# Kernel tuning notes

Measured on AMD Instinct MI355X. Metric: run time of the kernel, lower is better.

The kernel has to match this reference:

```python
import jax, jax.numpy as jnp
import numpy as np

D_MODEL, EDGE_DIM, HIDDEN = 128, 9, 256
B, N = 2, 512


def setup_inputs() -> dict:
    key = jax.random.key(0)
    ks = jax.random.split(key, 12)
    s = 0.05
    return {
        "z_prime": jax.random.normal(ks[0], (B, N, D_MODEL), jnp.float32),
        "edge_features": jax.random.normal(ks[1], (N, N, EDGE_DIM), jnp.float32),
        "candidate_edge_mask": jax.random.randint(ks[2], (N, N), 0, 2, jnp.int32),
        # organ head params (in, out) layout
        "Wo1": jax.random.normal(ks[3], (D_MODEL, HIDDEN), jnp.float32) * s,
        "bo1": jnp.zeros((HIDDEN,), jnp.float32),
        "Wo2": jax.random.normal(ks[4], (HIDDEN, 1), jnp.float32) * s,
        "bo2": jnp.zeros((1,), jnp.float32),
        # edge head first linear, split by input blocks [zi | zj | edge_feat]
        "We_i": jax.random.normal(ks[5], (D_MODEL, HIDDEN), jnp.float32) * s,
        "We_j": jax.random.normal(ks[6], (D_MODEL, HIDDEN), jnp.float32) * s,
        "We_e": jax.random.normal(ks[7], (EDGE_DIM, HIDDEN), jnp.float32) * s,
        "be1": jnp.zeros((HIDDEN,), jnp.float32),
        "We2": jax.random.normal(ks[8], (HIDDEN, 1), jnp.float32) * s,
        "be2": jnp.zeros((1,), jnp.float32),
    }


def reference(z_prime, edge_features, candidate_edge_mask,
              Wo1, bo1, Wo2, bo2, We_i, We_j, We_e, be1, We2, be2):
    # organ head: sigmoid(MLP(z)) -> (B, N)
    h_o = jax.nn.relu(jnp.einsum('bnd,dh->bnh', z_prime, Wo1) + bo1)
    organ_susceptibility = jax.nn.sigmoid(
        (jnp.einsum('bnh,ho->bno', h_o, Wo2) + bo2).squeeze(-1))

    # edge head: concat([zi, zj, E]) @ W1 decomposed into per-node/per-edge
    # projections (identical math to the concatenated linear).
    pi = jnp.einsum('bnd,dh->bnh', z_prime, We_i)   # (B, N, H) -> broadcast over j
    pj = jnp.einsum('bnd,dh->bnh', z_prime, We_j)   # (B, N, H) -> broadcast over i
    pe = jnp.einsum('ijd,dh->ijh', edge_features, We_e)  # (N, N, H)
    h = jax.nn.relu(pi[:, :, None, :] + pj[:, None, :, :] + pe[None] + be1)
    edge_prob = jax.nn.sigmoid(
        (jnp.einsum('bijh,ho->bijo', h, We2) + be2).squeeze(-1))
    edge_prob = edge_prob * candidate_edge_mask.astype(edge_prob.dtype)[None]
    return (organ_susceptibility, edge_prob)
```

## Files before the change

### kernel.cpp

```cpp
#include <hip/hip_runtime.h>
#include <math.h>
#include <stdint.h>

#define D_MODEL 128
#define EDGE_DIM 9
#define HIDDEN 256
#define BATCH 2
#define NN 512

#define TI 4
#define TJ 32

typedef _Float16 h2v    __attribute__((ext_vector_type(2)));
typedef __fp16   fp16x2 __attribute__((ext_vector_type(2)));
typedef _Float16 f16x8  __attribute__((ext_vector_type(8)));
typedef float    f32x4  __attribute__((ext_vector_type(4)));

struct H8 { h2v v[4]; };

__device__ __forceinline__ uint32_t h2u(h2v v) { return __builtin_bit_cast(uint32_t, v); }
__device__ __forceinline__ h2v u2h(uint32_t u) { return __builtin_bit_cast(h2v, u); }
__device__ __forceinline__ h2v pkrtz(float a, float b) {
    return __builtin_bit_cast(h2v, __builtin_amdgcn_cvt_pkrtz(a, b));
}
__device__ __forceinline__ h2v relu2(h2v v) {
    h2v z = {(_Float16)0.0f, (_Float16)0.0f};
    return __builtin_elementwise_max(v, z);
}
__device__ __forceinline__ float fdot2(h2v a, h2v b, float c) {
    return __builtin_amdgcn_fdot2(__builtin_bit_cast(fp16x2, a),
                                  __builtin_bit_cast(fp16x2, b), c, false);
}
__device__ __forceinline__ float sigmoidf_(float x) { return 1.f / (1.f + expf(-x)); }

__global__ __launch_bounds__(512) void node_mfma_kernel(
    const float* __restrict__ z,
    const float* __restrict__ Wo1,
    const float* __restrict__ bo1,
    const float* __restrict__ Wo2,
    const float* __restrict__ bo2,
    const float* __restrict__ We_i,
    const float* __restrict__ We_j,
    const float* __restrict__ be1,
    float* __restrict__ organ_out,
    uint32_t* __restrict__ pi_h,
    uint32_t* __restrict__ pj_h)
{
    __shared__ uint32_t Wlds[256][68];
    __shared__ float org_part[32][4];

    const int t    = threadIdx.x;
    const int lane = t & 63;
    const int wave = t >> 6;
    const int rb   = blockIdx.x;
    const int m    = blockIdx.y;

    const float* __restrict__ W = (m == 0) ? Wo1 : (m == 1) ? We_i : We_j;

    for (int idx = t; idx < 64 * 256; idx += 512) {
        const int d2 = idx >> 8;
        const int h  = idx & 255;
        const float wlo = W[(2 * d2) * 256 + h];
        const float whi = W[(2 * d2 + 1) * 256 + h];
        Wlds[h][d2 ^ ((h & 7) << 3)] = h2u(pkrtz(wlo, whi));
    }

    const int rt = wave & 1;
    const int cg = wave >> 1;
    const int kg = lane >> 4;
    const int row = rb * 32 + rt * 16 + (lane & 15);

    f16x8 A[4];
#pragma unroll
    for (int kt = 0; kt < 4; ++kt) {
        const float4 za = *(const float4*)&z[(size_t)row * 128 + kt * 32 + kg * 8];
        const float4 zb = *(const float4*)&z[(size_t)row * 128 + kt * 32 + kg * 8 + 4];
        H8 a;
        a.v[0] = pkrtz(za.x, za.y); a.v[1] = pkrtz(za.z, za.w);
        a.v[2] = pkrtz(zb.x, zb.y); a.v[3] = pkrtz(zb.z, zb.w);
        A[kt] = __builtin_bit_cast(f16x8, a);
    }

    __syncthreads();

    f32x4 C[4];
#pragma unroll
    for (int ct = 0; ct < 4; ++ct) {
        const int col = (cg * 4 + ct) * 16 + (lane & 15);
        C[ct] = (f32x4){0.f, 0.f, 0.f, 0.f};
#pragma unroll
        for (int kt = 0; kt < 4; ++kt) {
            const int d2b = (kt * 16 + kg * 4) ^ ((col & 7) << 3);
            const uint4 w = *(const uint4*)&Wlds[col][d2b];
            H8 b;
            b.v[0] = u2h(w.x); b.v[1] = u2h(w.y);
            b.v[2] = u2h(w.z); b.v[3] = u2h(w.w);
            C[ct] = __builtin_amdgcn_mfma_f32_16x16x32_f16(
                        A[kt], __builtin_bit_cast(f16x8, b), C[ct], 0, 0, 0);
        }
    }

    if (m == 0) {
        float s0 = 0.f, s1 = 0.f, s2 = 0.f, s3 = 0.f;
#pragma unroll
        for (int ct = 0; ct < 4; ++ct) {
            const int col = (cg * 4 + ct) * 16 + (lane & 15);
            const float b1 = bo1[col];
            const float w2 = Wo2[col];
            s0 = fmaf(fmaxf(C[ct].x + b1, 0.f), w2, s0);
            s1 = fmaf(fmaxf(C[ct].y + b1, 0.f), w2, s1);
            s2 = fmaf(fmaxf(C[ct].z + b1, 0.f), w2, s2);
            s3 = fmaf(fmaxf(C[ct].w + b1, 0.f), w2, s3);
        }
#pragma unroll
        for (int off = 1; off <= 8; off <<= 1) {
            s0 += __shfl_xor(s0, off, 64);
            s1 += __shfl_xor(s1, off, 64);
            s2 += __shfl_xor(s2, off, 64);
            s3 += __shfl_xor(s3, off, 64);
        }
        if ((lane & 15) == 0) {
            const int rbase = rt * 16 + kg * 4;
            org_part[rbase + 0][cg] = s0;
            org_part[rbase + 1][cg] = s1;
            org_part[rbase + 2][cg] = s2;
            org_part[rbase + 3][cg] = s3;
        }
        __syncthreads();
        if (t < 32) {
            const float s = org_part[t][0] + org_part[t][1]
                          + org_part[t][2] + org_part[t][3] + bo2[0];
            organ_out[rb * 32 + t] = sigmoidf_(s);
        }
    } else {
        uint32_t* __restrict__ dst = (m == 1) ? pi_h : pj_h;
        const bool addb = (m == 1);
#pragma unroll
        for (int ct = 0; ct < 4; ++ct) {
            const int col = (cg * 4 + ct) * 16 + (lane & 15);
            const float bv = addb ? be1[col] : 0.f;
            float v0 = C[ct].x + bv, v1 = C[ct].y + bv;
            float v2 = C[ct].z + bv, v3 = C[ct].w + bv;
            const float p0 = __shfl_xor(v0, 1, 64);
            const float p1 = __shfl_xor(v1, 1, 64);
            const float p2 = __shfl_xor(v2, 1, 64);
            const float p3 = __shfl_xor(v3, 1, 64);
            if (!(lane & 1)) {
                const int hp = col >> 1;
                const size_t gr = (size_t)(rb * 32 + rt * 16 + kg * 4);
                dst[(gr + 0) * 128 + hp] = h2u(pkrtz(v0, p0));
                dst[(gr + 1) * 128 + hp] = h2u(pkrtz(v1, p1));
                dst[(gr + 2) * 128 + hp] = h2u(pkrtz(v2, p2));
                dst[(gr + 3) * 128 + hp] = h2u(pkrtz(v3, p3));
            }
        }
    }
}

__global__ __launch_bounds__(256, 8) void edge_kernel(
    const float* __restrict__ E,
    const int*   __restrict__ mask,
    const float* __restrict__ We_e,
    const float* __restrict__ We2,
    const float* __restrict__ be2,
    const uint32_t* __restrict__ pi_h,
    const uint32_t* __restrict__ pj_h,
    float* __restrict__ edge_out)
{
    __shared__ __align__(16) uint32_t E_s[TI][TJ][12];
    __shared__ float sums_s[BATCH][TI][33];

    const int t    = threadIdx.x;
    const int lane = t & 63;
    const int wave = t >> 6;
    const int bi   = blockIdx.x;
    const int i0   = (bi >> 4) * TI;
    const int j0   = (bi & 15) * TJ;

#pragma unroll
    for (int ii = 0; ii < TI; ++ii) {
        const float* src = &E[((size_t)(i0 + ii) * NN + j0) * EDGE_DIM];
        for (int idx = t; idx < TJ * EDGE_DIM; idx += 256) {
            const int jl = idx / 9;
            const int d  = idx - jl * 9;
            const float e = src[idx];
            E_s[ii][jl][d] = h2u(pkrtz(e, e));
        }
    }

    h2v wee[EDGE_DIM][2];
    const float4* We_e4 = (const float4*)We_e;
#pragma unroll
    for (int d = 0; d < EDGE_DIM; ++d) {
        const float4 w = We_e4[d * 64 + lane];
        wee[d][0] = pkrtz(w.x, w.y);
        wee[d][1] = pkrtz(w.z, w.w);
    }
    h2v w2[2];
    {
        const float4 w = ((const float4*)We2)[lane];
        w2[0] = pkrtz(w.x, w.y);
        w2[1] = pkrtz(w.z, w.w);
    }

    h2v pir[BATCH][TI][2];
#pragma unroll
    for (int b = 0; b < BATCH; ++b)
#pragma unroll
        for (int ii = 0; ii < TI; ++ii) {
            const uint2 u = ((const uint2*)&pi_h[(size_t)(b * NN + i0 + ii) * 128])[lane];
            pir[b][ii][0] = u2h(u.x);
            pir[b][ii][1] = u2h(u.y);
        }

    __syncthreads();

    uint2 pjp[BATCH];
    {
        const int j = j0 + wave * 8;
        pjp[0] = ((const uint2*)&pj_h[(size_t)(0 * NN + j) * 128])[lane];
        pjp[1] = ((const uint2*)&pj_h[(size_t)(1 * NN + j) * 128])[lane];
    }

#pragma unroll
    for (int q = 0; q < 8; ++q) {
        const int jl = wave * 8 + q;

        h2v pjr[BATCH][2];
        pjr[0][0] = u2h(pjp[0].x); pjr[0][1] = u2h(pjp[0].y);
        pjr[1][0] = u2h(pjp[1].x); pjr[1][1] = u2h(pjp[1].y);

        if (q < 7) {
            const int j = j0 + jl + 1;
            pjp[0] = ((const uint2*)&pj_h[(size_t)(0 * NN + j) * 128])[lane];
            pjp[1] = ((const uint2*)&pj_h[(size_t)(1 * NN + j) * 128])[lane];
        }

        float vals[8];
#pragma unroll
        for (int ii = 0; ii < TI; ++ii) {
            const uint32_t* erow = &E_s[ii][jl][0];
            const uint4 ua = *(const uint4*)(erow);
            const uint4 ub = *(const uint4*)(erow + 4);
            const uint32_t uc = erow[8];

            h2v pe0, pe1;
            {
                const h2v e0 = u2h(ua.x), e1 = u2h(ua.y), e2 = u2h(ua.z), e3 = u2h(ua.w);
                const h2v e4 = u2h(ub.x), e5 = u2h(ub.y), e6 = u2h(ub.z), e7 = u2h(ub.w);
                const h2v e8 = u2h(uc);
                pe0 = e0 * wee[0][0];            pe1 = e0 * wee[0][1];
                pe0 = pe0 + e1 * wee[1][0];      pe1 = pe1 + e1 * wee[1][1];
                pe0 = pe0 + e2 * wee[2][0];      pe1 = pe1 + e2 * wee[2][1];
                pe0 = pe0 + e3 * wee[3][0];      pe1 = pe1 + e3 * wee[3][1];
                pe0 = pe0 + e4 * wee[4][0];      pe1 = pe1 + e4 * wee[4][1];
                pe0 = pe0 + e5 * wee[5][0];      pe1 = pe1 + e5 * wee[5][1];
                pe0 = pe0 + e6 * wee[6][0];      pe1 = pe1 + e6 * wee[6][1];
                pe0 = pe0 + e7 * wee[7][0];      pe1 = pe1 + e7 * wee[7][1];
                pe0 = pe0 + e8 * wee[8][0];      pe1 = pe1 + e8 * wee[8][1];
            }

#pragma unroll
            for (int b = 0; b < BATCH; ++b) {
                h2v v0 = relu2(pir[b][ii][0] + pjr[b][0] + pe0);
                h2v v1 = relu2(pir[b][ii][1] + pjr[b][1] + pe1);
                vals[2 * ii + b] = fdot2(v1, w2[1], fdot2(v0, w2[0], 0.f));
            }
        }

        float a0, a1, a2, a3;
        {
            const bool b0 = lane & 1;
            float k0 = b0 ? vals[1] : vals[0], s0 = b0 ? vals[0] : vals[1];
            float k1 = b0 ? vals[3] : vals[2], s1 = b0 ? vals[2] : vals[3];
            float k2 = b0 ? vals[5] : vals[4], s2 = b0 ? vals[4] : vals[5];
            float k3 = b0 ? vals[7] : vals[6], s3 = b0 ? vals[6] : vals[7];
            a0 = k0 + __shfl_xor(s0, 1, 64);
            a1 = k1 + __shfl_xor(s1, 1, 64);
            a2 = k2 + __shfl_xor(s2, 1, 64);
            a3 = k3 + __shfl_xor(s3, 1, 64);
        }
        {
            const bool b1 = (lane >> 1) & 1;
            float k0 = b1 ? a1 : a0, s0 = b1 ? a0 : a1;
            float k1 = b1 ? a3 : a2, s1 = b1 ? a2 : a3;
            a0 = k0 + __shfl_xor(s0, 2, 64);
            a1 = k1 + __shfl_xor(s1, 2, 64);
        }
        {
            const bool b2 = (lane >> 2) & 1;
            float k = b2 ? a1 : a0, s = b2 ? a0 : a1;
            a0 = k + __shfl_xor(s, 4, 64);
        }
        a0 += __shfl_xor(a0, 8, 64);
        a0 += __shfl_xor(a0, 16, 64);
        a0 += __shfl_xor(a0, 32, 64);

        if (lane < 8) sums_s[lane & 1][lane >> 1][jl] = a0;
    }
    __syncthreads();

    {
        const int b   = t >> 7;
        const int rem = t & 127;
        const int ii  = rem >> 5;
        const int jl  = rem & 31;
        const int i = i0 + ii, j = j0 + jl;
        const float s = sums_s[b][ii][jl] + be2[0];
        float p = sigmoidf_(s) * (float)mask[i * NN + j];
        edge_out[((size_t)b * NN + i) * NN + j] = p;
    }
}

extern "C" void kernel_launch(void* const* d_in, const int* in_sizes, int n_in,
                              void* d_out, int out_size, void* d_ws, size_t ws_size,
                              hipStream_t stream) {
    const float* z    = (const float*)d_in[0];
    const float* E    = (const float*)d_in[1];
    const int*   mask = (const int*)  d_in[2];
    const float* Wo1  = (const float*)d_in[3];
    const float* bo1  = (const float*)d_in[4];
    const float* Wo2  = (const float*)d_in[5];
    const float* bo2  = (const float*)d_in[6];
    const float* We_i = (const float*)d_in[7];
    const float* We_j = (const float*)d_in[8];
    const float* We_e = (const float*)d_in[9];
    const float* be1  = (const float*)d_in[10];
    const float* We2  = (const float*)d_in[11];
    const float* be2  = (const float*)d_in[12];

    float* out_organ = (float*)d_out;
    float* out_edge  = out_organ + BATCH * NN;

    uint32_t* pi_h = (uint32_t*)d_ws;
    uint32_t* pj_h = pi_h + (size_t)BATCH * NN * (HIDDEN/2);

    hipLaunchKernelGGL(node_mfma_kernel,
                       dim3(32, 3), dim3(512), 0, stream,
                       z, Wo1, bo1, Wo2, bo2, We_i, We_j, be1,
                       out_organ, pi_h, pj_h);

    hipLaunchKernelGGL(edge_kernel,
                       dim3((NN / TI) * (NN / TJ)), dim3(256), 0, stream,
                       E, mask, We_e, We2, be2, pi_h, pj_h, out_edge);
}
```

Baseline: 41.68 us.

## Map edge lanes to j with transposed pj, removing cross-lane reductions

The edge kernel is restructured so each lane owns one j column and loops over the hidden dimension, accumulating the output dot product in registers. The per-edge shuffle reduction across 64 lanes goes away. pj is written transposed (hidden-major) by the node kernel so lanes read consecutive j values coalesced. Weights and pi are staged in LDS, and tiles grow to 8x64 with lower occupancy bounds. Each lane now recomputes pe per hidden chunk, and pj is read strided from global memory for every hidden pair, so the memory-access pattern changes considerably.

```diff
diff --git a/kernel.cpp b/kernel.cpp
--- a/kernel.cpp
+++ b/kernel.cpp
@@ -8,9 +8,6 @@
 #define BATCH 2
 #define NN 512
 
-#define TI 4
-#define TJ 32
-
 typedef _Float16 h2v    __attribute__((ext_vector_type(2)));
 typedef __fp16   fp16x2 __attribute__((ext_vector_type(2)));
 typedef _Float16 f16x8  __attribute__((ext_vector_type(8)));
@@ -32,6 +29,9 @@
                                   __builtin_bit_cast(fp16x2, b), c, false);
 }
 __device__ __forceinline__ float sigmoidf_(float x) { return 1.f / (1.f + expf(-x)); }
+__device__ __forceinline__ uint32_t el(const uint4& u, int k) {
+    switch (k) { case 0: return u.x; case 1: return u.y; case 2: return u.z; default: return u.w; }
+}
 
 __global__ __launch_bounds__(512) void node_mfma_kernel(
     const float* __restrict__ z,
@@ -44,7 +44,7 @@
     const float* __restrict__ be1,
     float* __restrict__ organ_out,
     uint32_t* __restrict__ pi_h,
-    uint32_t* __restrict__ pj_h)
+    uint32_t* __restrict__ pj_T)
 {
     __shared__ uint32_t Wlds[256][68];
     __shared__ float org_part[32][4];
@@ -132,13 +132,11 @@
                           + org_part[t][2] + org_part[t][3] + bo2[0];
             organ_out[rb * 32 + t] = sigmoidf_(s);
         }
-    } else {
-        uint32_t* __restrict__ dst = (m == 1) ? pi_h : pj_h;
-        const bool addb = (m == 1);
+    } else if (m == 1) {
 #pragma unroll
         for (int ct = 0; ct < 4; ++ct) {
             const int col = (cg * 4 + ct) * 16 + (lane & 15);
-            const float bv = addb ? be1[col] : 0.f;
+            const float bv = be1[col];
             float v0 = C[ct].x + bv, v1 = C[ct].y + bv;
             float v2 = C[ct].z + bv, v3 = C[ct].w + bv;
             const float p0 = __shfl_xor(v0, 1, 64);
@@ -148,167 +146,158 @@
             if (!(lane & 1)) {
                 const int hp = col >> 1;
                 const size_t gr = (size_t)(rb * 32 + rt * 16 + kg * 4);
-                dst[(gr + 0) * 128 + hp] = h2u(pkrtz(v0, p0));
-                dst[(gr + 1) * 128 + hp] = h2u(pkrtz(v1, p1));
-                dst[(gr + 2) * 128 + hp] = h2u(pkrtz(v2, p2));
-                dst[(gr + 3) * 128 + hp] = h2u(pkrtz(v3, p3));
+                pi_h[(gr + 0) * 128 + hp] = h2u(pkrtz(v0, p0));
+                pi_h[(gr + 1) * 128 + hp] = h2u(pkrtz(v1, p1));
+                pi_h[(gr + 2) * 128 + hp] = h2u(pkrtz(v2, p2));
+                pi_h[(gr + 3) * 128 + hp] = h2u(pkrtz(v3, p3));
             }
         }
-    }
-}
-
-__global__ __launch_bounds__(256, 8) void edge_kernel(
+    } else {
+#pragma unroll
+        for (int ct = 0; ct < 4; ++ct) {
+            const int col = (cg * 4 + ct) * 16 + (lane & 15);
+            float v0 = C[ct].x, v1 = C[ct].y, v2 = C[ct].z, v3 = C[ct].w;
+            const float p0 = __shfl_xor(v0, 1, 64);
+            const float p1 = __shfl_xor(v1, 1, 64);
+            const float p2 = __shfl_xor(v2, 1, 64);
+            const float p3 = __shfl_xor(v3, 1, 64);
+            if (!(lane & 1)) {
+                const int hp = col >> 1;
+                const size_t gr = (size_t)(rb * 32 + rt * 16 + kg * 4);
+                pj_T[(size_t)hp * (BATCH * NN) + gr + 0] = h2u(pkrtz(v0, p0));
+                pj_T[(size_t)hp * (BATCH * NN) + gr + 1] = h2u(pkrtz(v1, p1));
+                pj_T[(size_t)hp * (BATCH * NN) + gr + 2] = h2u(pkrtz(v2, p2));
+                pj_T[(size_t)hp * (BATCH * NN) + gr + 3] = h2u(pkrtz(v3, p3));
+            }
+        }
+    }
+}
+
+__global__ __launch_bounds__(256, 4) void edge_kernel(
     const float* __restrict__ E,
     const int*   __restrict__ mask,
     const float* __restrict__ We_e,
     const float* __restrict__ We2,
     const float* __restrict__ be2,
     const uint32_t* __restrict__ pi_h,
-    const uint32_t* __restrict__ pj_h,
+    const uint32_t* __restrict__ pj_T,
     float* __restrict__ edge_out)
 {
-    __shared__ __align__(16) uint32_t E_s[TI][TJ][12];
-    __shared__ float sums_s[BATCH][TI][33];
+    __shared__ __align__(16) uint32_t E_s[8][64][12];
+    __shared__ __align__(16) uint32_t wee_s[EDGE_DIM][128];
+    __shared__ __align__(16) uint32_t we2_s[128];
+    __shared__ __align__(16) uint32_t pi_s[BATCH][8][128];
 
     const int t    = threadIdx.x;
     const int lane = t & 63;
-    const int wave = t >> 6;
+    const int w    = t >> 6;
     const int bi   = blockIdx.x;
-    const int i0   = (bi >> 4) * TI;
-    const int j0   = (bi & 15) * TJ;
-
-#pragma unroll
-    for (int ii = 0; ii < TI; ++ii) {
+    const int i0   = (bi >> 3) * 8;
+    const int j0   = (bi & 7) * 64;
+
+#pragma unroll
+    for (int ii = 0; ii < 8; ++ii) {
         const float* src = &E[((size_t)(i0 + ii) * NN + j0) * EDGE_DIM];
-        for (int idx = t; idx < TJ * EDGE_DIM; idx += 256) {
+        for (int idx = t; idx < 64 * EDGE_DIM; idx += 256) {
             const int jl = idx / 9;
             const int d  = idx - jl * 9;
             const float e = src[idx];
             E_s[ii][jl][d] = h2u(pkrtz(e, e));
         }
     }
-
-    h2v wee[EDGE_DIM][2];
-    const float4* We_e4 = (const float4*)We_e;
-#pragma unroll
-    for (int d = 0; d < EDGE_DIM; ++d) {
-        const float4 w = We_e4[d * 64 + lane];
-        wee[d][0] = pkrtz(w.x, w.y);
-        wee[d][1] = pkrtz(w.z, w.w);
-    }
-    h2v w2[2];
+    for (int idx = t; idx < EDGE_DIM * 128; idx += 256) {
+        const int d  = idx >> 7;
+        const int h2 = idx & 127;
+        wee_s[d][h2] = h2u(pkrtz(We_e[d * 256 + 2 * h2], We_e[d * 256 + 2 * h2 + 1]));
+    }
+    if (t < 128) we2_s[t] = h2u(pkrtz(We2[2 * t], We2[2 * t + 1]));
     {
-        const float4 w = ((const float4*)We2)[lane];
-        w2[0] = pkrtz(w.x, w.y);
-        w2[1] = pkrtz(w.z, w.w);
-    }
-
-    h2v pir[BATCH][TI][2];
-#pragma unroll
-    for (int b = 0; b < BATCH; ++b)
-#pragma unroll
-        for (int ii = 0; ii < TI; ++ii) {
-            const uint2 u = ((const uint2*)&pi_h[(size_t)(b * NN + i0 + ii) * 128])[lane];
-            pir[b][ii][0] = u2h(u.x);
-            pir[b][ii][1] = u2h(u.y);
-        }
-
+#pragma unroll
+        for (int k = 0; k < 2; ++k) {
+            const int idx = t + k * 256;
+            const int r16 = idx >> 5;
+            const int c4  = idx & 31;
+            const int b   = r16 >> 3;
+            const int il  = r16 & 7;
+            const uint4 v = *(const uint4*)&pi_h[(size_t)(b * NN + i0 + il) * 128 + c4 * 4];
+            *(uint4*)&pi_s[b][il][c4 * 4] = v;
+        }
+    }
     __syncthreads();
 
-    uint2 pjp[BATCH];
+    h2v e0[9], e1[9];
     {
-        const int j = j0 + wave * 8;
-        pjp[0] = ((const uint2*)&pj_h[(size_t)(0 * NN + j) * 128])[lane];
-        pjp[1] = ((const uint2*)&pj_h[(size_t)(1 * NN + j) * 128])[lane];
-    }
-
-#pragma unroll
-    for (int q = 0; q < 8; ++q) {
-        const int jl = wave * 8 + q;
-
-        h2v pjr[BATCH][2];
-        pjr[0][0] = u2h(pjp[0].x); pjr[0][1] = u2h(pjp[0].y);
-        pjr[1][0] = u2h(pjp[1].x); pjr[1][1] = u2h(pjp[1].y);
-
-        if (q < 7) {
-            const int j = j0 + jl + 1;
-            pjp[0] = ((const uint2*)&pj_h[(size_t)(0 * NN + j) * 128])[lane];
-            pjp[1] = ((const uint2*)&pj_h[(size_t)(1 * NN + j) * 128])[lane];
-        }
-
-        float vals[8];
-#pragma unroll
-        for (int ii = 0; ii < TI; ++ii) {
-            const uint32_t* erow = &E_s[ii][jl][0];
-            const uint4 ua = *(const uint4*)(erow);
-            const uint4 ub = *(const uint4*)(erow + 4);
-            const uint32_t uc = erow[8];
-
-            h2v pe0, pe1;
+        const uint32_t* r0 = &E_s[2 * w + 0][lane][0];
+        const uint4 a0 = *(const uint4*)(r0);
+        const uint4 b0 = *(const uint4*)(r0 + 4);
+        e0[0]=u2h(a0.x); e0[1]=u2h(a0.y); e0[2]=u2h(a0.z); e0[3]=u2h(a0.w);
+        e0[4]=u2h(b0.x); e0[5]=u2h(b0.y); e0[6]=u2h(b0.z); e0[7]=u2h(b0.w);
+        e0[8]=u2h(r0[8]);
+        const uint32_t* r1 = &E_s[2 * w + 1][lane][0];
+        const uint4 a1 = *(const uint4*)(r1);
+        const uint4 b1 = *(const uint4*)(r1 + 4);
+        e1[0]=u2h(a1.x); e1[1]=u2h(a1.y); e1[2]=u2h(a1.z); e1[3]=u2h(a1.w);
+        e1[4]=u2h(b1.x); e1[5]=u2h(b1.y); e1[6]=u2h(b1.z); e1[7]=u2h(b1.w);
+        e1[8]=u2h(r1[8]);
+    }
+
+    float acc[2][2] = {{0.f, 0.f}, {0.f, 0.f}};
+
+    const uint32_t* pjbase0 = pj_T + j0 + lane;
+    const uint32_t* pjbase1 = pj_T + NN + j0 + lane;
+
+    for (int hc = 0; hc < 128; hc += 4) {
+        uint4 wee4[EDGE_DIM];
+#pragma unroll
+        for (int d = 0; d < EDGE_DIM; ++d) wee4[d] = *(const uint4*)&wee_s[d][hc];
+        const uint4 we24 = *(const uint4*)&we2_s[hc];
+        uint4 pi4[2][2];
+#pragma unroll
+        for (int b = 0; b < 2; ++b) {
+            pi4[b][0] = *(const uint4*)&pi_s[b][2 * w + 0][hc];
+            pi4[b][1] = *(const uint4*)&pi_s[b][2 * w + 1][hc];
+        }
+        uint32_t pjv0[4], pjv1[4];
+#pragma unroll
+        for (int k = 0; k < 4; ++k) {
+            pjv0[k] = pjbase0[(size_t)(hc + k) * (BATCH * NN)];
+            pjv1[k] = pjbase1[(size_t)(hc + k) * (BATCH * NN)];
+        }
+
+#pragma unroll
+        for (int k = 0; k < 4; ++k) {
+            const h2v w2k = u2h(el(we24, k));
             {
-                const h2v e0 = u2h(ua.x), e1 = u2h(ua.y), e2 = u2h(ua.z), e3 = u2h(ua.w);
-                const h2v e4 = u2h(ub.x), e5 = u2h(ub.y), e6 = u2h(ub.z), e7 = u2h(ub.w);
-                const h2v e8 = u2h(uc);
-                pe0 = e0 * wee[0][0];            pe1 = e0 * wee[0][1];
-                pe0 = pe0 + e1 * wee[1][0];      pe1 = pe1 + e1 * wee[1][1];
-                pe0 = pe0 + e2 * wee[2][0];      pe1 = pe1 + e2 * wee[2][1];
-                pe0 = pe0 + e3 * wee[3][0];      pe1 = pe1 + e3 * wee[3][1];
-                pe0 = pe0 + e4 * wee[4][0];      pe1 = pe1 + e4 * wee[4][1];
-                pe0 = pe0 + e5 * wee[5][0];      pe1 = pe1 + e5 * wee[5][1];
-                pe0 = pe0 + e6 * wee[6][0];      pe1 = pe1 + e6 * wee[6][1];
-                pe0 = pe0 + e7 * wee[7][0];      pe1 = pe1 + e7 * wee[7][1];
-                pe0 = pe0 + e8 * wee[8][0];      pe1 = pe1 + e8 * wee[8][1];
+                h2v pe = e0[0] * u2h(el(wee4[0], k));
+#pragma unroll
+                for (int d = 1; d < EDGE_DIM; ++d) pe += e0[d] * u2h(el(wee4[d], k));
+                h2v t0 = relu2(pe + u2h(pjv0[k]) + u2h(el(pi4[0][0], k)));
+                acc[0][0] = fdot2(t0, w2k, acc[0][0]);
+                h2v t1 = relu2(pe + u2h(pjv1[k]) + u2h(el(pi4[1][0], k)));
+                acc[0][1] = fdot2(t1, w2k, acc[0][1]);
             }
-
-#pragma unroll
-            for (int b = 0; b < BATCH; ++b) {
-                h2v v0 = relu2(pir[b][ii][0] + pjr[b][0] + pe0);
-                h2v v1 = relu2(pir[b][ii][1] + pjr[b][1] + pe1);
-                vals[2 * ii + b] = fdot2(v1, w2[1], fdot2(v0, w2[0], 0.f));
+            {
+                h2v pe = e1[0] * u2h(el(wee4[0], k));
+#pragma unroll
+                for (int d = 1; d < EDGE_DIM; ++d) pe += e1[d] * u2h(el(wee4[d], k));
+                h2v t0 = relu2(pe + u2h(pjv0[k]) + u2h(el(pi4[0][1], k)));
+                acc[1][0] = fdot2(t0, w2k, acc[1][0]);
+                h2v t1 = relu2(pe + u2h(pjv1[k]) + u2h(el(pi4[1][1], k)));
+                acc[1][1] = fdot2(t1, w2k, acc[1][1]);
             }
         }
-
-        float a0, a1, a2, a3;
-        {
-            const bool b0 = lane & 1;
-            float k0 = b0 ? vals[1] : vals[0], s0 = b0 ? vals[0] : vals[1];
-            float k1 = b0 ? vals[3] : vals[2], s1 = b0 ? vals[2] : vals[3];
-            float k2 = b0 ? vals[5] : vals[4], s2 = b0 ? vals[4] : vals[5];
-            float k3 = b0 ? vals[7] : vals[6], s3 = b0 ? vals[6] : vals[7];
-            a0 = k0 + __shfl_xor(s0, 1, 64);
-            a1 = k1 + __shfl_xor(s1, 1, 64);
-            a2 = k2 + __shfl_xor(s2, 1, 64);
-            a3 = k3 + __shfl_xor(s3, 1, 64);
-        }
-        {
-            const bool b1 = (lane >> 1) & 1;
-            float k0 = b1 ? a1 : a0, s0 = b1 ? a0 : a1;
-            float k1 = b1 ? a3 : a2, s1 = b1 ? a2 : a3;
-            a0 = k0 + __shfl_xor(s0, 2, 64);
-            a1 = k1 + __shfl_xor(s1, 2, 64);
-        }
-        {
-            const bool b2 = (lane >> 2) & 1;
-            float k = b2 ? a1 : a0, s = b2 ? a0 : a1;
-            a0 = k + __shfl_xor(s, 4, 64);
-        }
-        a0 += __shfl_xor(a0, 8, 64);
-        a0 += __shfl_xor(a0, 16, 64);
-        a0 += __shfl_xor(a0, 32, 64);
-
-        if (lane < 8) sums_s[lane & 1][lane >> 1][jl] = a0;
-    }
-    __syncthreads();
-
-    {
-        const int b   = t >> 7;
-        const int rem = t & 127;
-        const int ii  = rem >> 5;
-        const int jl  = rem & 31;
-        const int i = i0 + ii, j = j0 + jl;
-        const float s = sums_s[b][ii][jl] + be2[0];
-        float p = sigmoidf_(s) * (float)mask[i * NN + j];
-        edge_out[((size_t)b * NN + i) * NN + j] = p;
+    }
+
+    const float b2 = be2[0];
+#pragma unroll
+    for (int ii = 0; ii < 2; ++ii) {
+        const int i = i0 + 2 * w + ii;
+        const float mv = (float)mask[(size_t)i * NN + j0 + lane];
+#pragma unroll
+        for (int b = 0; b < 2; ++b) {
+            const float s = acc[ii][b] + b2;
+            edge_out[((size_t)b * NN + i) * NN + j0 + lane] = sigmoidf_(s) * mv;
+        }
     }
 }
 
@@ -333,14 +322,14 @@
     float* out_edge  = out_organ + BATCH * NN;
 
     uint32_t* pi_h = (uint32_t*)d_ws;
-    uint32_t* pj_h = pi_h + (size_t)BATCH * NN * (HIDDEN/2);
+    uint32_t* pj_T = pi_h + (size_t)BATCH * NN * (HIDDEN/2);
 
     hipLaunchKernelGGL(node_mfma_kernel,
                        dim3(32, 3), dim3(512), 0, stream,
                        z, Wo1, bo1, Wo2, bo2, We_i, We_j, be1,
-                       out_organ, pi_h, pj_h);
+                       out_organ, pi_h, pj_T);
 
     hipLaunchKernelGGL(edge_kernel,
-                       dim3((NN / TI) * (NN / TJ)), dim3(256), 0, stream,
-                       E, mask, We_e, We2, be2, pi_h, pj_h, out_edge);
-}
+                       dim3(64 * 8), dim3(256), 0, stream,
+                       E, mask, We_e, We2, be2, pi_h, pj_T, out_edge);
+}
```

Result: slower. 42.78 us (+2.6%).
